# Optimization experiments

Measured on AMD Instinct MI355X. Metric: run time of the kernel, lower is better.

## Reference

```python
import jax, jax.numpy as jnp
import numpy as np

N_NODES = 2000
LN_EPS = 1e-5
NEG_SLOPE = 0.2  # PyG GATConv default


def _gat(xg, W, b, a_src, a_dst, src, dst):
    # xg: [G, N, Fin]; single-head GATConv, add_self_loops=False
    h = xg @ W                      # [G, N, H]
    es = h @ a_src                  # [G, N]
    ed = h @ a_dst                  # [G, N]
    e = jax.nn.leaky_relu(es[:, src] + ed[:, dst], NEG_SLOPE)  # [G, E]

    def seg_softmax(e_g):
        m = jax.ops.segment_max(e_g, dst, num_segments=N_NODES)
        ex = jnp.exp(e_g - m[dst])
        s = jax.ops.segment_sum(ex, dst, num_segments=N_NODES)
        return ex / (s[dst] + 1e-16)

    alpha = jax.vmap(seg_softmax)(e)            # [G, E]
    msg = alpha[..., None] * h[:, src]          # [G, E, H]
    agg = jax.vmap(lambda m_: jax.ops.segment_sum(m_, dst, num_segments=N_NODES))(msg)
    return agg + b                              # [G, N, H]


def _gcn_layer(x, W, b, a_src, a_dst, src, dst):
    # x: [B, N, T, F] -- faithfully replicate original permute + raw reshape
    B, N, T, F = x.shape
    x_in = jnp.transpose(x, (0, 2, 1, 3)).reshape(B * T, N, F)
    out = _gat(x_in, W, b, a_src, a_dst, src, dst)          # [B*T, N, H]
    out = jax.nn.gelu(out.reshape(B, T, N, -1), approximate=False)
    # original does .reshape(B, N, T, -1) on a [B,T,N,H]-contiguous tensor
    return out.reshape(B, N, T, -1)


def _lstm(x, Wih, Whh, bih, bhh):
    # x: [BN, T, Fin]; torch LSTM gate order i,f,g,o
    BN, T, _ = x.shape
    H = Whh.shape[1]
    xz = x @ Wih.T + (bih + bhh)                # [BN, T, 4H]

    def step(carry, z_t):
        h, c = carry
        z = z_t + h @ Whh.T
        i, f, g, o = jnp.split(z, 4, axis=-1)
        c = jax.nn.sigmoid(f) * c + jax.nn.sigmoid(i) * jnp.tanh(g)
        h = jax.nn.sigmoid(o) * jnp.tanh(c)
        return (h, c), h

    init = (jnp.zeros((BN, H), x.dtype), jnp.zeros((BN, H), x.dtype))
    _, hs = jax.lax.scan(step, init, jnp.swapaxes(xz, 0, 1))
    return jnp.swapaxes(hs, 0, 1)               # [BN, T, H]


def setup_inputs() -> dict:
    key = jax.random.key(0)
    ks = jax.random.split(key, 20)
    B, N, T, NX, H, PL, NY, E = 2, N_NODES, 24, 8, 64, 12, 1, 32000
    p = {}
    p["x"] = jax.random.normal(ks[0], (B, N, T, NX), jnp.float32)
    p["edge_src"] = jax.random.randint(ks[1], (E,), 0, N, jnp.int32)
    p["edge_dst"] = jax.random.randint(ks[2], (E,), 0, N, jnp.int32)
    p["fc_W"] = jax.random.normal(ks[3], (NX, H), jnp.float32) / np.sqrt(NX)
    p["fc_b"] = jnp.zeros((H,), jnp.float32)
    for i, tag in enumerate(["g1", "g2"]):
        p[f"{tag}_W"] = jax.random.normal(ks[4 + 4 * i], (H, H), jnp.float32) / np.sqrt(H)
        p[f"{tag}_b"] = jnp.zeros((H,), jnp.float32)
        p[f"{tag}_asrc"] = jax.random.normal(ks[5 + 4 * i], (H,), jnp.float32) / np.sqrt(H)
        p[f"{tag}_adst"] = jax.random.normal(ks[6 + 4 * i], (H,), jnp.float32) / np.sqrt(H)
    p["lstm_Wih"] = jax.random.normal(ks[12], (4 * H, H), jnp.float32) / np.sqrt(H)
    p["lstm_Whh"] = jax.random.normal(ks[13], (4 * H, H), jnp.float32) / np.sqrt(H)
    p["lstm_bih"] = jnp.zeros((4 * H,), jnp.float32)
    p["lstm_bhh"] = jnp.zeros((4 * H,), jnp.float32)
    p["ln_g"] = jnp.ones((H,), jnp.float32)
    p["ln_b"] = jnp.zeros((H,), jnp.float32)
    p["dense_W"] = jax.random.normal(ks[14], (H, PL * NY), jnp.float32) / np.sqrt(H)
    p["dense_b"] = jnp.zeros((PL * NY,), jnp.float32)
    return p


def reference(x, edge_src, edge_dst, fc_W, fc_b,
              g1_W, g1_b, g1_asrc, g1_adst,
              g2_W, g2_b, g2_asrc, g2_adst,
              lstm_Wih, lstm_Whh, lstm_bih, lstm_bhh,
              ln_g, ln_b, dense_W, dense_b):
    B, N, T, _ = x.shape
    PRED_LEN, NY = 12, 1
    x_h = x @ fc_W + fc_b                                        # [B,N,T,H]
    g1 = _gcn_layer(x_h, g1_W, g1_b, g1_asrc, g1_adst, edge_src, edge_dst)
    g2 = _gcn_layer(g1, g2_W, g2_b, g2_asrc, g2_adst, edge_src, edge_dst)
    H = g2.shape[-1]
    lout = _lstm(g2.reshape(B * N, T, -1), lstm_Wih, lstm_Whh, lstm_bih, lstm_bhh)
    lout = lout.reshape(B, N, T, H)
    mu = jnp.mean(lout, axis=-1, keepdims=True)
    var = jnp.mean(jnp.square(lout - mu), axis=-1, keepdims=True)
    h = (lout - mu) / jnp.sqrt(var + LN_EPS) * ln_g + ln_b
    out = h[:, :, -1:, :] @ dense_W + dense_b                    # [B,N,1,PL*NY]
    return out.reshape(B, N, PRED_LEN, NY)
```

## Files before the change

### kernel.cpp

```cpp
#include <hip/hip_runtime.h>
#include <hip/hip_bf16.h>
#include <math.h>

#define B_   2
#define N_   2000
#define T_   24
#define NX_  8
#define H_   64
#define G_   (B_*T_)
#define E_   32000
#define BN_  (B_*N_)
#define TH_  (T_*H_)
#define NTH_ (N_*T_*H_)
#define GNH_ (G_*N_*H_)
#define NPARAM_ 43340
#define NPARAM_PAD_ 43392
#define LSTM_PAD 72
#define DEGCAP 64

using bf16 = __hip_bfloat16;
typedef short bf16x8 __attribute__((ext_vector_type(8)));
typedef float f32x4  __attribute__((ext_vector_type(4)));

__device__ __forceinline__ float uasf(unsigned u){ return __uint_as_float(u); }
__device__ __forceinline__ float wave_sum(float v){
  #pragma unroll
  for (int o = 32; o > 0; o >>= 1) v += __shfl_xor(v, o, 64);
  return v;
}
__device__ __forceinline__ float half_sum(float v){
  #pragma unroll
  for (int o = 16; o > 0; o >>= 1) v += __shfl_xor(v, o, 64);
  return v;
}
__device__ __forceinline__ float half_max(float v){
  #pragma unroll
  for (int o = 16; o > 0; o >>= 1) v = fmaxf(v, __shfl_xor(v, o, 64));
  return v;
}
__device__ __forceinline__ float fastrcp(float x){ return __builtin_amdgcn_rcpf(x); }
__device__ __forceinline__ float sigf(float x){ return fastrcp(1.f + __expf(-x)); }
__device__ __forceinline__ float tanhfast(float x){ return 1.f - 2.f*fastrcp(1.f + __expf(2.f*x)); }
__device__ __forceinline__ float gelu_exact(float x){ return 0.5f*x*(1.f + erff(x*0.70710678118654752f)); }
__device__ __forceinline__ unsigned f2bf_rtn(float f){
  unsigned u = __float_as_uint(f);
  u += 0x7fffu + ((u >> 16) & 1u);
  return u >> 16;
}
__device__ __forceinline__ bf16x8 pack8(float4 a, float4 b){
  bf16x8 v;
  v[0]=(short)f2bf_rtn(a.x); v[1]=(short)f2bf_rtn(a.y);
  v[2]=(short)f2bf_rtn(a.z); v[3]=(short)f2bf_rtn(a.w);
  v[4]=(short)f2bf_rtn(b.x); v[5]=(short)f2bf_rtn(b.y);
  v[6]=(short)f2bf_rtn(b.z); v[7]=(short)f2bf_rtn(b.w);
  return v;
}

struct ConvArgs {
  const void* src[18];
  int off[19];
};
__global__ __launch_bounds__(256) void prep_kernel(
    ConvArgs a, const unsigned* __restrict__ xw,
    float* __restrict__ dst, int* __restrict__ flag,
    int* __restrict__ cnt_g,
    float* __restrict__ wc, float* __restrict__ bc){
  __shared__ int scnt;
  int tid = threadIdx.x;
  if (tid == 0) scnt = 0;
  __syncthreads();
  int c = 0;
  for (int i = tid; i < 4096; i += 256){
    unsigned e = (xw[i] >> 7) & 0xffu;
    if (e >= 100u && e <= 140u) c++;
  }
  atomicAdd(&scnt, c);
  __syncthreads();
  int isbf = (scnt > 3276) ? 1 : 0;
  int bid = blockIdx.x;

  if (bid < 170){
    if (bid == 0 && tid == 0) *flag = isbf;
    int i = bid*256 + tid;
    if (i < NPARAM_){
      int seg = 0;
      while (i >= a.off[seg+1]) seg++;
      int j = i - a.off[seg];
      float v;
      if (isbf) v = uasf(((unsigned)((const unsigned short*)a.src[seg])[j]) << 16);
      else      v = ((const float*)a.src[seg])[j];
      dst[i] = v;
    }
  } else if (bid == 170){
    for (int i = tid; i < N_; i += 256) cnt_g[i] = 0;
  } else {
    const void* pfcW = a.src[0];
    const void* pfcb = a.src[1];
    const void* pg1W = a.src[2];
    #pragma unroll
    for (int half = 0; half < 2; ++half){
      int t2 = half*256 + tid;
      int i = t2 >> 6, n = t2 & 63;
      float s = 0.f;
      #pragma unroll
      for (int k = 0; k < 64; ++k){
        float fa = isbf ? uasf(((unsigned)((const unsigned short*)pfcW)[i*64+k]) << 16)
                        : ((const float*)pfcW)[i*64+k];
        float fb = isbf ? uasf(((unsigned)((const unsigned short*)pg1W)[k*64+n]) << 16)
                        : ((const float*)pg1W)[k*64+n];
        s = fmaf(fa, fb, s);
      }
      wc[i*64 + n] = s;
    }
    if (tid < 64){
      float b = 0.f;
      #pragma unroll
      for (int k = 0; k < 64; ++k){
        float fa = isbf ? uasf(((unsigned)((const unsigned short*)pfcb)[k]) << 16)
                        : ((const float*)pfcb)[k];
        float fb = isbf ? uasf(((unsigned)((const unsigned short*)pg1W)[k*64+tid]) << 16)
                        : ((const float*)pg1W)[k*64+tid];
        b = fmaf(fa, fb, b);
      }
      bc[tid] = b;
    }
  }
}

__global__ __launch_bounds__(256) void gat_h1_fused_kernel(
    const void* __restrict__ xraw, const int* __restrict__ flag,
    const int* __restrict__ esrc, const int* __restrict__ edst,
    int* __restrict__ cnt_g, int* __restrict__ slot,
    const float* __restrict__ wc, const float* __restrict__ bc,
    const float* __restrict__ asrc, const float* __restrict__ adst,
    unsigned short* __restrict__ hbuf, float* __restrict__ es, float* __restrict__ ed){
  if (blockIdx.x < 125){
    int e = blockIdx.x*256 + threadIdx.x;
    int d = edst[e];
    int pos = atomicAdd(&cnt_g[d], 1);
    if (pos < DEGCAP) slot[(d << 6) + pos] = esrc[e];
  }
  int lane = threadIdx.x & 63, wave = threadIdx.x >> 6;
  int q = lane >> 4, c = lane & 15;
  int isbf = *flag;
  bf16x8 Bf[4];
  #pragma unroll
  for (int nt = 0; nt < 4; ++nt){
    bf16x8 v;
    #pragma unroll
    for (int j = 0; j < 8; ++j)
      v[j] = (q == 0) ? (short)f2bf_rtn(wc[j*64 + nt*16 + c]) : (short)0;
    Bf[nt] = v;
  }
  float bcv[4];
  #pragma unroll
  for (int nt = 0; nt < 4; ++nt) bcv[nt] = bc[nt*16 + c];
  float aS[4], aD[4];
  #pragma unroll
  for (int nt = 0; nt < 4; ++nt){ aS[nt] = asrc[nt*16+c]; aD[nt] = adst[nt*16+c]; }

  int w = blockIdx.x*4 + wave;
  #pragma unroll
  for (int it = 0; it < 2; ++it){
    int tile = w*2 + it;
    int p0 = tile*16;
    int g  = p0 / N_, n0 = p0 - g*N_;
    int bb = g / T_,  tt = g - bb*T_;
    bf16x8 A0;
    #pragma unroll
    for (int j = 0; j < 8; ++j) A0[j] = 0;
    if (q == 0){
      size_t rowelt = ((size_t)(bb*N_ + n0 + c)*T_ + tt)*NX_;
      if (isbf){
        A0 = *(const bf16x8*)((const unsigned short*)xraw + rowelt);
      } else {
        const float4* xr4 = (const float4*)((const float*)xraw + rowelt);
        A0 = pack8(xr4[0], xr4[1]);
      }
    }
    f32x4 acc[4];
    #pragma unroll
    for (int nt = 0; nt < 4; ++nt){ acc[nt][0]=bcv[nt]; acc[nt][1]=bcv[nt]; acc[nt][2]=bcv[nt]; acc[nt][3]=bcv[nt]; }
    #pragma unroll
    for (int nt = 0; nt < 4; ++nt) acc[nt] = __builtin_amdgcn_mfma_f32_16x16x32_bf16(A0, Bf[nt], acc[nt], 0, 0, 0);

    #pragma unroll
    for (int nt = 0; nt < 4; ++nt){
      #pragma unroll
      for (int r = 0; r < 4; ++r)
        hbuf[(size_t)(p0 + q*4 + r)*H_ + nt*16 + c] = (unsigned short)f2bf_rtn(acc[nt][r]);
    }
    #pragma unroll
    for (int r = 0; r < 4; ++r){
      float e1 = acc[0][r]*aS[0] + acc[1][r]*aS[1] + acc[2][r]*aS[2] + acc[3][r]*aS[3];
      float e2 = acc[0][r]*aD[0] + acc[1][r]*aD[1] + acc[2][r]*aD[2] + acc[3][r]*aD[3];
      #pragma unroll
      for (int o = 8; o > 0; o >>= 1){
        e1 += __shfl_xor(e1, o, 64);
        e2 += __shfl_xor(e2, o, 64);
      }
      if (c == 0){
        es[p0 + q*4 + r] = e1;
        ed[p0 + q*4 + r] = e2;
      }
    }
  }
}

__global__ __launch_bounds__(256) void gat_h2_mfma_kernel(
    const float* __restrict__ xin, const float* __restrict__ W,
    const float* __restrict__ asrc, const float* __restrict__ adst,
    unsigned short* __restrict__ hbuf, float* __restrict__ es, float* __restrict__ ed){
  int lane = threadIdx.x & 63, wave = threadIdx.x >> 6;
  int q = lane >> 4, c = lane & 15;
  bf16x8 Bf[4][2];
  #pragma unroll
  for (int nt = 0; nt < 4; ++nt){
    #pragma unroll
    for (int ks = 0; ks < 2; ++ks){
      bf16x8 v;
      #pragma unroll
      for (int j = 0; j < 8; ++j)
        v[j] = (short)f2bf_rtn(W[(ks*32 + q*8 + j)*H_ + nt*16 + c]);
      Bf[nt][ks] = v;
    }
  }
  float aS[4], aD[4];
  #pragma unroll
  for (int nt = 0; nt < 4; ++nt){ aS[nt] = asrc[nt*16+c]; aD[nt] = adst[nt*16+c]; }

  int w = blockIdx.x*4 + wave;
  #pragma unroll
  for (int it = 0; it < 2; ++it){
    int tile = w*2 + it;
    int p0 = tile*16;
    int p  = p0 + c;
    int g = p / N_, n = p - g*N_;
    int bb = g / T_, t = g - bb*T_;
    const float4* xr4 = (const float4*)(xin + (size_t)bb*NTH_ + (size_t)n*TH_ + (size_t)t*H_);
    float4 x0 = xr4[q*2],     x1 = xr4[q*2 + 1];
    float4 x2 = xr4[8 + q*2], x3 = xr4[8 + q*2 + 1];
    bf16x8 A0 = pack8(x0, x1);
    bf16x8 A1 = pack8(x2, x3);

    f32x4 acc[4];
    #pragma unroll
    for (int nt = 0; nt < 4; ++nt){ acc[nt][0]=0.f; acc[nt][1]=0.f; acc[nt][2]=0.f; acc[nt][3]=0.f; }
    #pragma unroll
    for (int nt = 0; nt < 4; ++nt) acc[nt] = __builtin_amdgcn_mfma_f32_16x16x32_bf16(A0, Bf[nt][0], acc[nt], 0, 0, 0);
    #pragma unroll
    for (int nt = 0; nt < 4; ++nt) acc[nt] = __builtin_amdgcn_mfma_f32_16x16x32_bf16(A1, Bf[nt][1], acc[nt], 0, 0, 0);

    #pragma unroll
    for (int nt = 0; nt < 4; ++nt){
      #pragma unroll
      for (int r = 0; r < 4; ++r)
        hbuf[(size_t)(p0 + q*4 + r)*H_ + nt*16 + c] = (unsigned short)f2bf_rtn(acc[nt][r]);
    }
    #pragma unroll
    for (int r = 0; r < 4; ++r){
      float e1 = acc[0][r]*aS[0] + acc[1][r]*aS[1] + acc[2][r]*aS[2] + acc[3][r]*aS[3];
      float e2 = acc[0][r]*aD[0] + acc[1][r]*aD[1] + acc[2][r]*aD[2] + acc[3][r]*aD[3];
      #pragma unroll
      for (int o = 8; o > 0; o >>= 1){
        e1 += __shfl_xor(e1, o, 64);
        e2 += __shfl_xor(e2, o, 64);
      }
      if (c == 0){
        es[p0 + q*4 + r] = e1;
        ed[p0 + q*4 + r] = e2;
      }
    }
  }
}

__global__ __launch_bounds__(256) void gat_agg_kernel(
    const unsigned short* __restrict__ hbuf, const float* __restrict__ es, const float* __restrict__ ed,
    const int* __restrict__ cnt_g, const int* __restrict__ slot,
    const float* __restrict__ bias, float* __restrict__ gout){
  int lane = threadIdx.x & 63, wave = threadIdx.x >> 6;
  int h = lane >> 5, ln = lane & 31;
  int gd = (blockIdx.x*4 + wave)*2 + h;
  int g = gd / N_, d = gd - g*N_;
  int start = d << 6;
  int deg = min(cnt_g[d], DEGCAP);
  const float* esg = es + (size_t)g*N_;
  float edv = ed[(size_t)g*N_ + d];
  const char* hg = (const char*)(hbuf + (size_t)g*N_*H_);
  unsigned lanoff = ((unsigned)ln) << 2;
  int hbase = h << 5;
  int dm = max(deg, __shfl_xor(deg, 32, 64));

  float acc0 = 0.f, acc1 = 0.f;
  if (dm <= 32){
    int sv = 0; float sc = -1e30f;
    if (ln < deg){
      sv = slot[start + ln];
      float e = esg[sv] + edv;
      sc = e > 0.f ? e : 0.2f*e;
    }
    float m = half_max(sc);
    float ex = (ln < deg) ? __expf(sc - m) : 0.f;
    float ssum = half_sum(ex);
    ex *= fastrcp(ssum + 1e-16f);
    unsigned pw = (f2bf_rtn(ex) << 16) | (unsigned)sv;
    for (int j0 = 0; j0 < dm; j0 += 8){
      unsigned wv[8]; float aa[8]; unsigned off[8];
      #pragma unroll
      for (int u = 0; u < 8; ++u){
        int j = j0 + u;
        wv[u] = (unsigned)__shfl((int)pw, hbase + j, 64);
        aa[u] = (j < deg) ? uasf(wv[u] & 0xffff0000u) : 0.f;
        off[u] = ((wv[u] & 0xffffu) << 7) + lanoff;
      }
      unsigned hv[8];
      #pragma unroll
      for (int u = 0; u < 8; ++u)
        hv[u] = *(const unsigned*)(hg + off[u]);
      #pragma unroll
      for (int u = 0; u < 8; ++u){
        acc0 = fmaf(aa[u], uasf(hv[u] << 16), acc0);
        acc1 = fmaf(aa[u], uasf(hv[u] & 0xffff0000u), acc1);
      }
    }
  } else {
    float m = -1e30f;
    for (int base = 0; base < deg; base += 32){
      int i = base + ln;
      if (i < deg){
        int s = slot[start + i];
        float e = esg[s] + edv;
        float t = e > 0.f ? e : 0.2f*e;
        m = fmaxf(m, t);
      }
    }
    m = half_max(m);
    float ssum = 0.f;
    for (int base = 0; base < deg; base += 32){
      int i = base + ln;
      if (i < deg){
        int s = slot[start + i];
        float e = esg[s] + edv;
        float t = e > 0.f ? e : 0.2f*e;
        ssum += __expf(t - m);
      }
    }
    ssum = half_sum(ssum);
    float inv = fastrcp(ssum + 1e-16f);
    for (int base = 0; base < dm; base += 32){
      int i = base + ln;
      int sv = 0; float ex = 0.f;
      if (i < deg){
        sv = slot[start + i];
        float e = esg[sv] + edv;
        float t = e > 0.f ? e : 0.2f*e;
        ex = __expf(t - m) * inv;
      }
      unsigned pw = (f2bf_rtn(ex) << 16) | (unsigned)sv;
      int rem = dm - base; if (rem > 32) rem = 32;
      int myrem = deg - base;
      for (int j0 = 0; j0 < rem; j0 += 8){
        unsigned wv[8]; float aa[8]; unsigned off[8];
        #pragma unroll
        for (int u = 0; u < 8; ++u){
          int j = j0 + u;
          wv[u] = (unsigned)__shfl((int)pw, hbase + j, 64);
          aa[u] = (j < myrem) ? uasf(wv[u] & 0xffff0000u) : 0.f;
          off[u] = ((wv[u] & 0xffffu) << 7) + lanoff;
        }
        unsigned hv[8];
        #pragma unroll
        for (int u = 0; u < 8; ++u)
          hv[u] = *(const unsigned*)(hg + off[u]);
        #pragma unroll
        for (int u = 0; u < 8; ++u){
          acc0 = fmaf(aa[u], uasf(hv[u] << 16), acc0);
          acc1 = fmaf(aa[u], uasf(hv[u] & 0xffff0000u), acc1);
        }
      }
    }
  }
  float2 bv = ((const float2*)bias)[ln];
  float2 o2;
  o2.x = gelu_exact(acc0 + bv.x);
  o2.y = gelu_exact(acc1 + bv.y);
  ((float2*)(gout + (size_t)gd*H_))[ln] = o2;
}

__global__ __launch_bounds__(256) void lstm_final_kernel(
    const float* __restrict__ xin,
    const float* __restrict__ Wih,
    const float* __restrict__ Whh,
    const float* __restrict__ bih, const float* __restrict__ bhh,
    const float* __restrict__ lng, const float* __restrict__ lnb,
    const float* __restrict__ dW, const float* __restrict__ db,
    const int* __restrict__ flag, void* __restrict__ outv){
  __shared__ __align__(16) unsigned short Hlds[16*LSTM_PAD];
  __shared__ float smH[16][68];
  int tid = threadIdx.x;
  int lane = tid & 63, wave = tid >> 6;
  int q = lane >> 4, c = lane & 15;
  int s0 = blockIdx.x * 16;

  bf16x8 Bf[4][4];
  #pragma unroll
  for (int g = 0; g < 4; ++g){
    int n = g*64 + wave*16 + c;
    #pragma unroll
    for (int ks = 0; ks < 4; ++ks){
      const float* srcp = (ks < 2) ? (Whh + (size_t)n*64 + ks*32 + q*8)
                                   : (Wih + (size_t)n*64 + (ks-2)*32 + q*8);
      float4 a = ((const float4*)srcp)[0];
      float4 b = ((const float4*)srcp)[1];
      Bf[g][ks] = pack8(a, b);
    }
  }
  float bsum[4];
  #pragma unroll
  for (int g = 0; g < 4; ++g){
    int n = g*64 + wave*16 + c;
    bsum[g] = bih[n] + bhh[n];
  }
  for (int i = tid; i < 16*LSTM_PAD; i += 256) Hlds[i] = 0;
  float cst[4] = {0.f, 0.f, 0.f, 0.f};
  __syncthreads();

  for (int t = 0; t < T_; ++t){
    const float4* xr4 = (const float4*)(xin + ((size_t)(s0 + c)*T_ + t)*64);
    float4 x0 = xr4[q*2],     x1 = xr4[q*2 + 1];
    float4 x2 = xr4[8 + q*2], x3 = xr4[8 + q*2 + 1];
    bf16x8 Ax0 = pack8(x0, x1);
    bf16x8 Ax1 = pack8(x2, x3);
    const bf16x8* hrow = (const bf16x8*)(Hlds + c*LSTM_PAD);
    bf16x8 Ah0 = hrow[q];
    bf16x8 Ah1 = hrow[4 + q];

    f32x4 acc[4];
    #pragma unroll
    for (int g = 0; g < 4; ++g){ acc[g][0]=bsum[g]; acc[g][1]=bsum[g]; acc[g][2]=bsum[g]; acc[g][3]=bsum[g]; }
    #pragma unroll
    for (int g = 0; g < 4; ++g) acc[g] = __builtin_amdgcn_mfma_f32_16x16x32_bf16(Ah0, Bf[g][0], acc[g], 0, 0, 0);
    #pragma unroll
    for (int g = 0; g < 4; ++g) acc[g] = __builtin_amdgcn_mfma_f32_16x16x32_bf16(Ah1, Bf[g][1], acc[g], 0, 0, 0);
    #pragma unroll
    for (int g = 0; g < 4; ++g) acc[g] = __builtin_amdgcn_mfma_f32_16x16x32_bf16(Ax0, Bf[g][2], acc[g], 0, 0, 0);
    #pragma unroll
    for (int g = 0; g < 4; ++g) acc[g] = __builtin_amdgcn_mfma_f32_16x16x32_bf16(Ax1, Bf[g][3], acc[g], 0, 0, 0);

    float hv[4];
    #pragma unroll
    for (int r = 0; r < 4; ++r){
      float zi = acc[0][r], zf = acc[1][r], zg = acc[2][r], zo = acc[3][r];
      cst[r] = sigf(zf)*cst[r] + sigf(zi)*tanhfast(zg);
      hv[r] = sigf(zo)*tanhfast(cst[r]);
    }
    if (t == T_-1){
      #pragma unroll
      for (int r = 0; r < 4; ++r)
        smH[q*4 + r][wave*16 + c] = hv[r];
    } else {
      __syncthreads();
      #pragma unroll
      for (int r = 0; r < 4; ++r)
        Hlds[(q*4 + r)*LSTM_PAD + wave*16 + c] = (unsigned short)f2bf_rtn(hv[r]);
      __syncthreads();
    }
  }
  __syncthreads();

  int isbf = *flag;
  #pragma unroll
  for (int si = 0; si < 4; ++si){
    int s = wave*4 + si;
    float h = smH[s][lane];
    float mu = wave_sum(h) * (1.f/64.f);
    float dev = h - mu;
    float var = wave_sum(dev*dev) * (1.f/64.f);
    float hn = dev * rsqrtf(var + 1e-5f) * lng[lane] + lnb[lane];
    smH[s][lane] = hn;
    if (lane < 12){
      float o = db[lane];
      #pragma unroll
      for (int k = 0; k < 64; ++k) o = fmaf(smH[s][k], dW[k*12 + lane], o);
      size_t oi = (size_t)(s0 + s)*12 + lane;
      if (isbf) ((unsigned short*)outv)[oi] = (unsigned short)f2bf_rtn(o);
      else      ((float*)outv)[oi] = o;
    }
  }
}

extern "C" void kernel_launch(void* const* d_in, const int* in_sizes, int n_in,
                              void* d_out, int out_size, void* d_ws, size_t ws_size,
                              hipStream_t stream) {
  const int* esrc = (const int*)d_in[1];
  const int* edst = (const int*)d_in[2];

  static const int sizes[18] = {512, 64, 4096, 64, 64, 64, 4096, 64, 64, 64,
                                16384, 16384, 256, 256, 64, 64, 768, 12};
  static const int srcidx[18] = {3, 4, 5, 6, 7, 8, 9, 10, 11, 12,
                                 13, 14, 15, 16, 17, 18, 19, 20};
  ConvArgs ca;
  {
    int acc = 0;
    for (int i = 0; i < 18; ++i){ ca.src[i] = d_in[srcidx[i]]; ca.off[i] = acc; acc += sizes[i]; }
    ca.off[18] = acc;
  }

  float* P     = (float*)d_ws;
  float* bufA  = P + NPARAM_PAD_;
  float* bufB  = bufA + (size_t)GNH_;
  float* esb   = bufB + (size_t)GNH_;
  float* edb   = esb  + (size_t)G_*N_;
  int*   cnt_g = (int*)(edb + (size_t)G_*N_);
  int*   slot  = cnt_g + N_;
  int*   flag  = slot + N_*DEGCAP;
  float* wcb   = (float*)(flag + 1);
  unsigned short* hbuf = (unsigned short*)bufB;

  const float* pg1b = P + 4672;
  const float* pg1as= P + 4736;
  const float* pg1ad= P + 4800;
  const float* pg2W = P + 4864;
  const float* pg2b = P + 8960;
  const float* pg2as= P + 9024;
  const float* pg2ad= P + 9088;
  const float* pWih = P + 9152;
  const float* pWhh = P + 25536;
  const float* pbih = P + 41920;
  const float* pbhh = P + 42176;
  const float* plng = P + 42432;
  const float* plnb = P + 42496;
  const float* pdW  = P + 42560;
  const float* pdb  = P + 43328;

  prep_kernel<<<172, 256, 0, stream>>>(ca, (const unsigned*)d_in[0],
                                       P, flag, cnt_g, wcb, wcb + 512);

  gat_h1_fused_kernel<<<750, 256, 0, stream>>>(d_in[0], flag, esrc, edst, cnt_g, slot,
                                               wcb, wcb + 512, pg1as, pg1ad, hbuf, esb, edb);
  gat_agg_kernel<<<12000, 256, 0, stream>>>(hbuf, esb, edb, cnt_g, slot, pg1b, bufA);

  gat_h2_mfma_kernel<<<750, 256, 0, stream>>>(bufA, pg2W, pg2as, pg2ad, hbuf, esb, edb);
  gat_agg_kernel<<<12000, 256, 0, stream>>>(hbuf, esb, edb, cnt_g, slot, pg2b, bufA);

  lstm_final_kernel<<<250, 256, 0, stream>>>(bufA, pWih, pWhh, pbih, pbhh,
                                             plng, plnb, pdW, pdb, flag, d_out);
}
```

Measured before the change: 247.1 us.

## Process four destination nodes per wave with 8-byte gathers in GAT aggregation

The GAT aggregation kernel now assigns 16 lanes per destination node, so each wave handles four nodes instead of two. Each lane gathers 8 bytes (four bf16 features) per neighbour instead of 4. The softmax over up to 64 neighbours is held in registers in four chunks, which replaces the separate small- and large-degree paths. The grid is halved to match. This cuts the number of waves and widens each memory access, in exchange for more registers per lane and more shuffle rounds when degree is high.

```diff
diff --git a/kernel.cpp b/kernel.cpp
--- a/kernel.cpp
+++ b/kernel.cpp
@@ -26,16 +26,6 @@
 __device__ __forceinline__ float wave_sum(float v){
   #pragma unroll
   for (int o = 32; o > 0; o >>= 1) v += __shfl_xor(v, o, 64);
-  return v;
-}
-__device__ __forceinline__ float half_sum(float v){
-  #pragma unroll
-  for (int o = 16; o > 0; o >>= 1) v += __shfl_xor(v, o, 64);
-  return v;
-}
-__device__ __forceinline__ float half_max(float v){
-  #pragma unroll
-  for (int o = 16; o > 0; o >>= 1) v = fmaxf(v, __shfl_xor(v, o, 64));
   return v;
 }
 __device__ __forceinline__ float fastrcp(float x){ return __builtin_amdgcn_rcpf(x); }
@@ -279,112 +269,89 @@
     const int* __restrict__ cnt_g, const int* __restrict__ slot,
     const float* __restrict__ bias, float* __restrict__ gout){
   int lane = threadIdx.x & 63, wave = threadIdx.x >> 6;
-  int h = lane >> 5, ln = lane & 31;
-  int gd = (blockIdx.x*4 + wave)*2 + h;
+  int qd = lane >> 4, ln = lane & 15;
+  int gd = (blockIdx.x*4 + wave)*4 + qd;
   int g = gd / N_, d = gd - g*N_;
   int start = d << 6;
   int deg = min(cnt_g[d], DEGCAP);
   const float* esg = es + (size_t)g*N_;
   float edv = ed[(size_t)g*N_ + d];
   const char* hg = (const char*)(hbuf + (size_t)g*N_*H_);
-  unsigned lanoff = ((unsigned)ln) << 2;
-  int hbase = h << 5;
-  int dm = max(deg, __shfl_xor(deg, 32, 64));
-
-  float acc0 = 0.f, acc1 = 0.f;
-  if (dm <= 32){
-    int sv = 0; float sc = -1e30f;
-    if (ln < deg){
-      sv = slot[start + ln];
-      float e = esg[sv] + edv;
-      sc = e > 0.f ? e : 0.2f*e;
-    }
-    float m = half_max(sc);
-    float ex = (ln < deg) ? __expf(sc - m) : 0.f;
-    float ssum = half_sum(ex);
-    ex *= fastrcp(ssum + 1e-16f);
-    unsigned pw = (f2bf_rtn(ex) << 16) | (unsigned)sv;
-    for (int j0 = 0; j0 < dm; j0 += 8){
+  unsigned lanoff = ((unsigned)ln) << 3;
+  int hbase = qd << 4;
+  int dm = deg;
+  dm = max(dm, __shfl_xor(dm, 16, 64));
+  dm = max(dm, __shfl_xor(dm, 32, 64));
+  int NC = (dm + 15) >> 4;
+
+  int svk[4]; float sck[4];
+  #pragma unroll
+  for (int k = 0; k < 4; ++k){ svk[k] = 0; sck[k] = -1e30f; }
+  #pragma unroll
+  for (int k = 0; k < 4; ++k){
+    int i = k*16 + ln;
+    if (k < NC && i < deg) svk[k] = slot[start + i];
+  }
+  #pragma unroll
+  for (int k = 0; k < 4; ++k){
+    int i = k*16 + ln;
+    if (k < NC && i < deg){
+      float e = esg[svk[k]] + edv;
+      sck[k] = e > 0.f ? e : 0.2f*e;
+    }
+  }
+  float m = fmaxf(fmaxf(sck[0], sck[1]), fmaxf(sck[2], sck[3]));
+  #pragma unroll
+  for (int o = 8; o > 0; o >>= 1) m = fmaxf(m, __shfl_xor(m, o, 64));
+  float exk[4]; float ssum = 0.f;
+  #pragma unroll
+  for (int k = 0; k < 4; ++k){
+    int i = k*16 + ln;
+    float e = (k < NC && i < deg) ? __expf(sck[k] - m) : 0.f;
+    exk[k] = e; ssum += e;
+  }
+  #pragma unroll
+  for (int o = 8; o > 0; o >>= 1) ssum += __shfl_xor(ssum, o, 64);
+  float inv = fastrcp(ssum + 1e-16f);
+  unsigned pwk[4];
+  #pragma unroll
+  for (int k = 0; k < 4; ++k)
+    pwk[k] = (f2bf_rtn(exk[k]*inv) << 16) | (unsigned)svk[k];
+
+  float a0 = 0.f, a1 = 0.f, a2 = 0.f, a3 = 0.f;
+  for (int k = 0; k < NC; ++k){
+    unsigned pw = pwk[k];
+    int myrem = deg - k*16;
+    int remw = dm - k*16; if (remw > 16) remw = 16;
+    for (int j0 = 0; j0 < remw; j0 += 8){
       unsigned wv[8]; float aa[8]; unsigned off[8];
       #pragma unroll
       for (int u = 0; u < 8; ++u){
         int j = j0 + u;
         wv[u] = (unsigned)__shfl((int)pw, hbase + j, 64);
-        aa[u] = (j < deg) ? uasf(wv[u] & 0xffff0000u) : 0.f;
+        aa[u] = (j < myrem) ? uasf(wv[u] & 0xffff0000u) : 0.f;
         off[u] = ((wv[u] & 0xffffu) << 7) + lanoff;
       }
-      unsigned hv[8];
+      uint2 hv[8];
       #pragma unroll
       for (int u = 0; u < 8; ++u)
-        hv[u] = *(const unsigned*)(hg + off[u]);
+        hv[u] = *(const uint2*)(hg + off[u]);
       #pragma unroll
       for (int u = 0; u < 8; ++u){
-        acc0 = fmaf(aa[u], uasf(hv[u] << 16), acc0);
-        acc1 = fmaf(aa[u], uasf(hv[u] & 0xffff0000u), acc1);
-      }
-    }
-  } else {
-    float m = -1e30f;
-    for (int base = 0; base < deg; base += 32){
-      int i = base + ln;
-      if (i < deg){
-        int s = slot[start + i];
-        float e = esg[s] + edv;
-        float t = e > 0.f ? e : 0.2f*e;
-        m = fmaxf(m, t);
-      }
-    }
-    m = half_max(m);
-    float ssum = 0.f;
-    for (int base = 0; base < deg; base += 32){
-      int i = base + ln;
-      if (i < deg){
-        int s = slot[start + i];
-        float e = esg[s] + edv;
-        float t = e > 0.f ? e : 0.2f*e;
-        ssum += __expf(t - m);
-      }
-    }
-    ssum = half_sum(ssum);
-    float inv = fastrcp(ssum + 1e-16f);
-    for (int base = 0; base < dm; base += 32){
-      int i = base + ln;
-      int sv = 0; float ex = 0.f;
-      if (i < deg){
-        sv = slot[start + i];
-        float e = esg[sv] + edv;
-        float t = e > 0.f ? e : 0.2f*e;
-        ex = __expf(t - m) * inv;
-      }
-      unsigned pw = (f2bf_rtn(ex) << 16) | (unsigned)sv;
-      int rem = dm - base; if (rem > 32) rem = 32;
-      int myrem = deg - base;
-      for (int j0 = 0; j0 < rem; j0 += 8){
-        unsigned wv[8]; float aa[8]; unsigned off[8];
-        #pragma unroll
-        for (int u = 0; u < 8; ++u){
-          int j = j0 + u;
-          wv[u] = (unsigned)__shfl((int)pw, hbase + j, 64);
-          aa[u] = (j < myrem) ? uasf(wv[u] & 0xffff0000u) : 0.f;
-          off[u] = ((wv[u] & 0xffffu) << 7) + lanoff;
-        }
-        unsigned hv[8];
-        #pragma unroll
-        for (int u = 0; u < 8; ++u)
-          hv[u] = *(const unsigned*)(hg + off[u]);
-        #pragma unroll
-        for (int u = 0; u < 8; ++u){
-          acc0 = fmaf(aa[u], uasf(hv[u] << 16), acc0);
-          acc1 = fmaf(aa[u], uasf(hv[u] & 0xffff0000u), acc1);
-        }
-      }
-    }
-  }
-  float2 bv = ((const float2*)bias)[ln];
-  float2 o2;
-  o2.x = gelu_exact(acc0 + bv.x);
-  o2.y = gelu_exact(acc1 + bv.y);
-  ((float2*)(gout + (size_t)gd*H_))[ln] = o2;
+        a0 = fmaf(aa[u], uasf(hv[u].x << 16), a0);
+        a1 = fmaf(aa[u], uasf(hv[u].x & 0xffff0000u), a1);
+        a2 = fmaf(aa[u], uasf(hv[u].y << 16), a2);
+        a3 = fmaf(aa[u], uasf(hv[u].y & 0xffff0000u), a3);
+      }
+    }
+  }
+  float4 bv = ((const float4*)bias)[ln];
+  float4 o4;
+  o4.x = gelu_exact(a0 + bv.x);
+  o4.y = gelu_exact(a1 + bv.y);
+  o4.z = gelu_exact(a2 + bv.z);
+  o4.w = gelu_exact(a3 + bv.w);
+  ((float4*)(gout + (size_t)gd*H_))[ln] = o4;
 }
 
 __global__ __launch_bounds__(256) void lstm_final_kernel(
@@ -538,10 +505,10 @@
 
   gat_h1_fused_kernel<<<750, 256, 0, stream>>>(d_in[0], flag, esrc, edst, cnt_g, slot,
                                                wcb, wcb + 512, pg1as, pg1ad, hbuf, esb, edb);
-  gat_agg_kernel<<<12000, 256, 0, stream>>>(hbuf, esb, edb, cnt_g, slot, pg1b, bufA);
+  gat_agg_kernel<<<6000, 256, 0, stream>>>(hbuf, esb, edb, cnt_g, slot, pg1b, bufA);
 
   gat_h2_mfma_kernel<<<750, 256, 0, stream>>>(bufA, pg2W, pg2as, pg2ad, hbuf, esb, edb);
-  gat_agg_kernel<<<12000, 256, 0, stream>>>(hbuf, esb, edb, cnt_g, slot, pg2b, bufA);
+  gat_agg_kernel<<<6000, 256, 0, stream>>>(hbuf, esb, edb, cnt_g, slot, pg2b, bufA);
 
   lstm_final_kernel<<<250, 256, 0, stream>>>(bufA, pWih, pWhh, pbih, pbhh,
                                              plng, plnb, pdW, pdb, flag, d_out);
```

After: 233.2 us. 1.06x faster.
